# Optimization experiments

Hardware: AMD Instinct MI355X
Metric: run time of the kernel (lower is better)

Reference implementation:

```python
import jax, jax.numpy as jnp
import numpy as np

NR, NA = 2, 1                 # num_raw, num_angle
QDIM = NR + 2 * NA            # 4: [r, x1=cos(th), x2=sin(th)]
DQ = NR + NA                  # 3: [dr, dth]
D = 2 * NR + 3 * NA           # 7: full state dim
HID = 256
EPS = 1e-6


def setup_inputs() -> dict:
    key = jax.random.key(0)
    ks = jax.random.split(key, 4)
    B = 32768
    x = jax.random.normal(ks[0], (B, D), dtype=jnp.float32)
    W0 = jax.random.normal(ks[1], (HID, D), dtype=jnp.float32) / np.sqrt(D)
    b0 = jnp.zeros((HID,), dtype=jnp.float32)
    W1 = jax.random.normal(ks[2], (HID, HID), dtype=jnp.float32) / np.sqrt(HID)
    b1 = jnp.zeros((HID,), dtype=jnp.float32)
    W2 = jax.random.normal(ks[3], (1, HID), dtype=jnp.float32) / np.sqrt(HID)
    b2 = jnp.zeros((1,), dtype=jnp.float32)
    return {"x": x, "W0": W0, "b0": b0, "W1": W1, "b1": b1, "W2": W2, "b2": b2}


def _lnn_forward(x, W0, b0, W1, b1, W2, b2):
    def L_single(xi):  # scalar Lagrangian of one state (D,)
        h = jnp.tanh(W0 @ xi + b0)
        h = jnp.tanh(W1 @ h + b1)
        return (W2 @ h + b2)[0]

    grad_single = jax.grad(L_single)
    gradL = jax.vmap(grad_single)(x)                       # (B, D)

    # Rows of the Hessian corresponding to d/d(dr,dth): (B, DQ, D).
    # Replaces the torch per-row autograd.grad loop with one batched jacfwd.
    def g(xi):
        return grad_single(xi)[QDIM:]                      # dL/d(dr,dth), (DQ,)
    Hrows = jax.vmap(jax.jacfwd(g))(x)                     # (B, DQ, D)

    x1 = x[:, NR:NR + NA]                                  # cos part (B, NA)
    x2 = x[:, NR + NA:QDIM]                                # sin part (B, NA)

    Jr = Hrows[:, :, :NR]                                  # (B, DQ, NR)
    Jx1 = Hrows[:, :, NR:NR + NA]                          # (B, DQ, NA)
    Jx2 = Hrows[:, :, NR + NA:QDIM]                        # (B, DQ, NA)
    Hdq = Hrows[:, :, QDIM:] + EPS * jnp.eye(DQ, dtype=x.dtype)  # (B, DQ, DQ)

    # chain rule back to angle theta: d/dth = -x2 * d/dx1 + x1 * d/dx2
    Jth = -x2[:, None, :] * Jx1 + x1[:, None, :] * Jx2     # (B, DQ, NA)
    Jrth = jnp.concatenate([Jr, Jth], axis=2)              # (B, DQ, DQ)

    dLdr = gradL[:, :NR]
    dLdx1 = gradL[:, NR:NR + NA]
    dLdx2 = gradL[:, NR + NA:QDIM]
    dLdth = -x2 * dLdx1 + x1 * dLdx2
    dLdrdth = jnp.concatenate([dLdr, dLdth], axis=1)       # (B, DQ)

    dq = x[:, QDIM:]                                       # (B, DQ)
    dq_term = jnp.einsum('bij,bj->bi', Jrth, dq)

    rhs = dLdrdth - dq_term                                # control = 0 (no controlNet)
    ddq = jnp.linalg.solve(Hdq, rhs[..., None])[..., 0]    # (B, DQ)

    dr = dq[:, :NR]
    dth = dq[:, NR:]
    dx1 = -x2 * dth
    dx2 = x1 * dth
    return jnp.concatenate([dr, dx1, dx2, ddq], axis=1)    # (B, D)


def reference(x, W0, b0, W1, b1, W2, b2):
    return _lnn_forward(x, W0, b0, W1, b1, W2, b2)
```

## Files before the change

kernel.cpp:

```cpp
#include <hip/hip_runtime.h>
#include <math.h>

#define HID 256
#define EPS_REG 1e-6

typedef __attribute__((ext_vector_type(8))) short short8;
typedef __attribute__((ext_vector_type(4))) short short4v;
typedef __attribute__((ext_vector_type(4))) float v4f;

#define MFMA_BF16(a, b, c) __builtin_amdgcn_mfma_f32_16x16x32_bf16((a), (b), (c), 0, 0, 0)

__device__ __forceinline__ float fast_tanh(float z) {
    const float e = __expf(2.0f * z);
    const float d = e + 1.0f;
    float r = __builtin_amdgcn_rcpf(d);
    r = r * (2.0f - d * r);
    return fmaf(-2.0f, r, 1.0f);
}

__device__ __forceinline__ float rtn_bf16(float v, short* s) {
    unsigned r = (__float_as_uint(v) + 0x8000u) & 0xFFFF0000u;
    *s = (short)(r >> 16);
    return __uint_as_float(r);
}
__device__ __forceinline__ void split3(float v, short* a, short* b, short* c) {
    float f0 = rtn_bf16(v, a);
    float r1 = v - f0;
    float f1 = rtn_bf16(r1, b);
    float r2 = r1 - f1;
    (void)rtn_bf16(r2, c);
}

__global__ void prep_w1_frags(const float* __restrict__ W1, short* __restrict__ ws) {
    const int gid   = blockIdx.x * 128 + threadIdx.x;
    const int lane  = gid & 63;
    const int ks    = (gid >> 6) & 7;
    const int rt    = (gid >> 9) & 15;
    const int which = gid >> 13;
    const int m = lane & 15, q = lane >> 4;

    float v[8];
    if (which == 0) {
        const float* p = W1 + (size_t)(rt*16 + m)*HID + ks*32 + q*8;
        const float4 va = *(const float4*)(p);
        const float4 vb = *(const float4*)(p + 4);
        v[0]=va.x; v[1]=va.y; v[2]=va.z; v[3]=va.w;
        v[4]=vb.x; v[5]=vb.y; v[6]=vb.z; v[7]=vb.w;
    } else {
        const float* p = W1 + (size_t)(ks*32 + q*8)*HID + rt*16 + m;
#pragma unroll
        for (int t = 0; t < 8; ++t) v[t] = p[(size_t)t*HID];
    }
    short8 h8, m8, l8;
#pragma unroll
    for (int t = 0; t < 8; ++t) {
        short sh, sm, sl;
        split3(v[t], &sh, &sm, &sl);
        h8[t] = sh; m8[t] = sm; l8[t] = sl;
    }
    const size_t base = (size_t)which*3*65536 + ((size_t)(rt*8 + ks)*64 + lane)*8;
    *(short8*)(ws + base)          = h8;
    *(short8*)(ws + base + 65536)  = m8;
    *(short8*)(ws + base + 131072) = l8;
}

#define FRAG_NT_STRIDE 13056
#define FRAG_BUF_STRIDE 4352
#define BFRAG_SHORTS 26112
#define M0H_FLOATS 2304
#define PIPE_LDS_BYTES 122880

__device__ __forceinline__ void lnn_phase0(const float* __restrict__ x,
    const float* __restrict__ W0, const float* __restrict__ b0,
    int samp_base, short* __restrict__ Bf, float* __restrict__ M0, int tid)
{
    const int j  = tid & 255;
    const int s0 = (tid >> 8) * 4;
    float w0r[7];
#pragma unroll
    for (int d = 0; d < 7; ++d) w0r[d] = W0[j*7 + d];
    const float bj = b0[j];
    const int kbase = (j >> 3)*136 + (j & 7);
#pragma unroll
    for (int si = 0; si < 4; ++si) {
        const int s = s0 + si;
        const float* xs = x + (size_t)(samp_base + s)*7;
        float z = bj;
#pragma unroll
        for (int d = 0; d < 7; ++d) z = fmaf(w0r[d], xs[d], z);
        const float h  = fast_tanh(z);
        const float sg = 1.0f - h*h;
        M0[j*9 + s] = h;
        const int nt = s >> 2;
        const int cb = (s & 3) * 4;
        float vals[4] = {h, sg*w0r[4], sg*w0r[5], sg*w0r[6]};
#pragma unroll
        for (int comp = 0; comp < 4; ++comp) {
            short sh, sm, sl;
            split3(vals[comp], &sh, &sm, &sl);
            const int a = nt*FRAG_NT_STRIDE + kbase + (cb + comp)*8;
            Bf[a]                     = sh;
            Bf[a + FRAG_BUF_STRIDE]   = sm;
            Bf[a + 2*FRAG_BUF_STRIDE] = sl;
        }
    }
}

__device__ __forceinline__ void lnn_mm(const short8* __restrict__ Ah,
    const short8* __restrict__ Am, const short8* __restrict__ Al,
    const short* __restrict__ Bf, int w, int lane, int boff, v4f acc[2][2])
{
    short8 pah[2][2], pam[2][2], pal[2][2];
#pragma unroll
    for (int rtl = 0; rtl < 2; ++rtl) {
        const size_t fi = ((size_t)((w*2 + rtl)*8))*64 + lane;
        pah[0][rtl] = Ah[fi]; pam[0][rtl] = Am[fi]; pal[0][rtl] = Al[fi];
    }
#pragma unroll
    for (int ks = 0; ks < 8; ++ks) {
        const int cur = ks & 1, nxt = cur ^ 1;
        if (ks < 7) {
#pragma unroll
            for (int rtl = 0; rtl < 2; ++rtl) {
                const size_t fi = ((size_t)((w*2 + rtl)*8 + ks + 1))*64 + lane;
                pah[nxt][rtl] = Ah[fi]; pam[nxt][rtl] = Am[fi]; pal[nxt][rtl] = Al[fi];
            }
        }
        short8 bh[2], bm[2], bl[2];
#pragma unroll
        for (int nt = 0; nt < 2; ++nt) {
            const int a = nt*FRAG_NT_STRIDE + ks*544 + boff;
            bh[nt] = *(const short8*)(&Bf[a]);
            bm[nt] = *(const short8*)(&Bf[a + FRAG_BUF_STRIDE]);
            bl[nt] = *(const short8*)(&Bf[a + 2*FRAG_BUF_STRIDE]);
        }
#pragma unroll
        for (int rtl = 0; rtl < 2; ++rtl) {
            const short8 ah = pah[cur][rtl];
            const short8 am = pam[cur][rtl];
            const short8 al = pal[cur][rtl];
#pragma unroll
            for (int nt = 0; nt < 2; ++nt) {
                acc[rtl][nt] = MFMA_BF16(ah, bl[nt], acc[rtl][nt]);
                acc[rtl][nt] = MFMA_BF16(al, bh[nt], acc[rtl][nt]);
                acc[rtl][nt] = MFMA_BF16(am, bm[nt], acc[rtl][nt]);
                acc[rtl][nt] = MFMA_BF16(am, bh[nt], acc[rtl][nt]);
                acc[rtl][nt] = MFMA_BF16(ah, bm[nt], acc[rtl][nt]);
                acc[rtl][nt] = MFMA_BF16(ah, bh[nt], acc[rtl][nt]);
            }
        }
    }
}

__device__ __forceinline__ void lnn_epi1(v4f acc[2][2], short* __restrict__ Bf,
    const float* __restrict__ b1, const float* __restrict__ W2,
    int w, int lane, int q, int c)
{
    const int myreg = c & 3;
#pragma unroll
    for (int rtl = 0; rtl < 2; ++rtl) {
        const int base = (w*2 + rtl)*16;
        float b1r[4], w2r[4];
#pragma unroll
        for (int r = 0; r < 4; ++r) {
            b1r[r] = b1[base + q*4 + r];
            w2r[r] = W2[base + q*4 + r];
        }
        const int G  = (base >> 3) + (q >> 1);
        const int tq = (q & 1) * 4;
#pragma unroll
        for (int nt = 0; nt < 2; ++nt) {
            short4v ph, pm, pl;
#pragma unroll
            for (int r = 0; r < 4; ++r) {
                const float z0 = __shfl(acc[rtl][nt][r] + b1r[r], lane & ~3, 64);
                const float h1 = fast_tanh(z0);
                const float s1 = 1.0f - h1*h1;
                const float av = acc[rtl][nt][r];
                const float u  = (myreg == 0) ? (w2r[r]*s1)
                                              : (-2.0f*w2r[r]*h1*s1)*av;
                short sh, sm, sl;
                split3(u, &sh, &sm, &sl);
                ph[r] = sh; pm[r] = sm; pl[r] = sl;
            }
            const int a = nt*FRAG_NT_STRIDE + G*136 + c*8 + tq;
            *(short4v*)(&Bf[a])                     = ph;
            *(short4v*)(&Bf[a + FRAG_BUF_STRIDE])   = pm;
            *(short4v*)(&Bf[a + 2*FRAG_BUF_STRIDE]) = pl;
        }
    }
}

__device__ __forceinline__ void lnn_epi2(v4f acc2[2][2], short* __restrict__ Bf,
    const float* __restrict__ M0, const float* __restrict__ W0,
    int w, int lane, int q, int c)
{
    float* U0 = (float*)Bf;
#pragma unroll
    for (int rtl = 0; rtl < 2; ++rtl) {
#pragma unroll
        for (int reg = 0; reg < 4; ++reg) {
            const int j = (w*2 + rtl)*16 + q*4 + reg;
            const float w0sel = W0[j*7 + 3 + (c & 3)];
#pragma unroll
            for (int nt = 0; nt < 2; ++nt) {
                const int s = nt*4 + (c >> 2);
                const float pv = acc2[rtl][nt][reg];
                const float p0 = __shfl(pv, lane & ~3, 64);
                const float h0 = M0[j*9 + s];
                const float sg = 1.0f - h0*h0;
                const float t2 = -2.0f * p0 * h0 * sg;
                const float res = ((c & 3) == 0) ? (p0*sg)
                                                 : fmaf(pv, sg, t2 * w0sel);
                U0[j*36 + s*4 + (c & 3)] = res;
            }
        }
    }
}

__device__ __forceinline__ void lnn_phase3(const float* __restrict__ x,
    const float* __restrict__ W0, short* __restrict__ Bf,
    int samp_base, float* __restrict__ out, int w, int tid)
{
    const float* U0 = (const float*)Bf;
    float* scratch = ((float*)Bf) + 9216 + w * 425;
    const int t = tid & 63;
    float part[25];
#pragma unroll
    for (int qq = 0; qq < 25; ++qq) part[qq] = 0.0f;

#pragma unroll
    for (int m = 0; m < 4; ++m) {
        const int j = t + 64*m;
        const float4 uv = *(const float4*)(&U0[j*36 + w*4]);
        float w0d[7];
#pragma unroll
        for (int d = 0; d < 7; ++d) w0d[d] = W0[j*7 + d];
#pragma unroll
        for (int d = 0; d < 4; ++d) part[d] = fmaf(uv.x, w0d[d], part[d]);
#pragma unroll
        for (int d = 0; d < 7; ++d) {
            part[4  + d] = fmaf(uv.y, w0d[d], part[4  + d]);
            part[11 + d] = fmaf(uv.z, w0d[d], part[11 + d]);
            part[18 + d] = fmaf(uv.w, w0d[d], part[18 + d]);
        }
    }
#pragma unroll
    for (int off = 1; off <= 2; off <<= 1)
#pragma unroll
        for (int qq = 0; qq < 25; ++qq)
            part[qq] += __shfl_xor(part[qq], off, 64);
    {
        const int quad = t >> 2;
        if ((t & 3) == 0) {
#pragma unroll
            for (int e = 0; e < 25; ++e)
                scratch[e*17 + quad] = part[e];
        }
    }
    if (t < 25) {
        float tot = 0.0f;
#pragma unroll
        for (int k = 0; k < 16; ++k) tot += scratch[t*17 + k];
        scratch[t*17 + 16] = tot;
    }

    if (t == 0) {
        double g[25];
#pragma unroll
        for (int e = 0; e < 25; ++e) g[e] = (double)scratch[e*17 + 16];

        const float* xs = x + (size_t)(samp_base + w)*7;
        const double x1 = xs[2], x2 = xs[3];
        const double dq0 = xs[4], dq1 = xs[5], dth = xs[6];

        double M[3][3], rhs[3];
#pragma unroll
        for (int i = 0; i < 3; ++i) {
            const double J0 = g[4 + i*7 + 0];
            const double J1 = g[4 + i*7 + 1];
            const double J2 = -x2*g[4 + i*7 + 2] + x1*g[4 + i*7 + 3];
            const double dL = (i == 0) ? g[0]
                            : (i == 1) ? g[1]
                            : (-x2*g[2] + x1*g[3]);
            M[i][0] = g[4 + i*7 + 4] + (i == 0 ? EPS_REG : 0.0);
            M[i][1] = g[4 + i*7 + 5] + (i == 1 ? EPS_REG : 0.0);
            M[i][2] = g[4 + i*7 + 6] + (i == 2 ? EPS_REG : 0.0);
            rhs[i]  = dL - (J0*dq0 + J1*dq1 + J2*dth);
        }
        const double c00 = M[1][1]*M[2][2] - M[1][2]*M[2][1];
        const double c01 = M[1][2]*M[2][0] - M[1][0]*M[2][2];
        const double c02 = M[1][0]*M[2][1] - M[1][1]*M[2][0];
        const double det = M[0][0]*c00 + M[0][1]*c01 + M[0][2]*c02;
        const double inv = 1.0 / det;
        const double c10 = M[0][2]*M[2][1] - M[0][1]*M[2][2];
        const double c11 = M[0][0]*M[2][2] - M[0][2]*M[2][0];
        const double c12 = M[0][1]*M[2][0] - M[0][0]*M[2][1];
        const double c20 = M[0][1]*M[1][2] - M[0][2]*M[1][1];
        const double c21 = M[0][2]*M[1][0] - M[0][0]*M[1][2];
        const double c22 = M[0][0]*M[1][1] - M[0][1]*M[1][0];
        const double sol0 = (c00*rhs[0] + c10*rhs[1] + c20*rhs[2]) * inv;
        const double sol1 = (c01*rhs[0] + c11*rhs[1] + c21*rhs[2]) * inv;
        const double sol2 = (c02*rhs[0] + c12*rhs[1] + c22*rhs[2]) * inv;

        float* o = out + (size_t)(samp_base + w)*7;
        o[0] = (float)dq0;
        o[1] = (float)dq1;
        o[2] = (float)(-x2*dth);
        o[3] = (float)( x1*dth);
        o[4] = (float)sol0;
        o[5] = (float)sol1;
        o[6] = (float)sol2;
    }
}

__global__ __launch_bounds__(1024, 4)
void lnn_pipe(const float* __restrict__ x,
              const float* __restrict__ W0, const float* __restrict__ b0,
              const float* __restrict__ b1, const float* __restrict__ W2,
              const short* __restrict__ ws,
              float* __restrict__ out)
{
    extern __shared__ __align__(16) short smem[];

    const int tid  = threadIdx.x;
    const int w16  = tid >> 6;
    const int isA  = (w16 < 8) ? 1 : 0;
    const int w    = w16 & 7;
    const int lane = tid & 63;
    const int gtid = w*64 + lane;

    short* Bf = smem + (isA ? 0 : BFRAG_SHORTS);
    float* M0 = (float*)(smem + 2*BFRAG_SHORTS) + (isA ? 0 : M0H_FLOATS);
    const int samp0 = blockIdx.x * 16 + (isA ? 0 : 8);

    const short8* A1h = (const short8*)ws;
    const short8* A1m = A1h + 8192;
    const short8* A1l = A1h + 16384;
    const short8* A2h = A1h + 24576;
    const short8* A2m = A1h + 32768;
    const short8* A2l = A1h + 40960;

    const int q = lane >> 4;
    const int c = lane & 15;
    const int boff = q*136 + c*8;

    if (isA) lnn_phase0(x, W0, b0, samp0, Bf, M0, gtid);
    __syncthreads();

    v4f acc[2][2];
#pragma unroll
    for (int r = 0; r < 2; ++r)
#pragma unroll
        for (int n = 0; n < 2; ++n) acc[r][n] = (v4f){0.f, 0.f, 0.f, 0.f};
    if (isA) lnn_mm(A1h, A1m, A1l, Bf, w, lane, boff, acc);
    else     lnn_phase0(x, W0, b0, samp0, Bf, M0, gtid);
    __syncthreads();

    if (isA) lnn_epi1(acc, Bf, b1, W2, w, lane, q, c);
    else     lnn_mm(A1h, A1m, A1l, Bf, w, lane, boff, acc);
    __syncthreads();

    v4f acc2[2][2];
#pragma unroll
    for (int r = 0; r < 2; ++r)
#pragma unroll
        for (int n = 0; n < 2; ++n) acc2[r][n] = (v4f){0.f, 0.f, 0.f, 0.f};
    if (isA) lnn_mm(A2h, A2m, A2l, Bf, w, lane, boff, acc2);
    else     lnn_epi1(acc, Bf, b1, W2, w, lane, q, c);
    __syncthreads();

    if (isA) lnn_epi2(acc2, Bf, M0, W0, w, lane, q, c);
    else     lnn_mm(A2h, A2m, A2l, Bf, w, lane, boff, acc2);
    __syncthreads();

    if (isA) lnn_phase3(x, W0, Bf, samp0, out, w, gtid);
    else     lnn_epi2(acc2, Bf, M0, W0, w, lane, q, c);
    __syncthreads();

    if (!isA) lnn_phase3(x, W0, Bf, samp0, out, w, gtid);
}

__global__ __launch_bounds__(512, 4)
void lnn_mfma(const float* __restrict__ x,
              const float* __restrict__ W0, const float* __restrict__ b0,
              const float* __restrict__ b1, const float* __restrict__ W2,
              const short* __restrict__ ws,
              float* __restrict__ out)
{
    __shared__ __align__(16) short Bfrag[26112];
    __shared__ float M0h[HID * 9];

    const int tid   = threadIdx.x;
    const int samp0 = blockIdx.x * 8;
    const int lane  = tid & 63;
    const int w     = tid >> 6;

    lnn_phase0(x, W0, b0, samp0, Bfrag, M0h, tid);
    __syncthreads();

    const short8* A1h = (const short8*)ws;
    const short8* A1m = A1h + 8192;
    const short8* A1l = A1h + 16384;
    const short8* A2h = A1h + 24576;
    const short8* A2m = A1h + 32768;
    const short8* A2l = A1h + 40960;

    const int q = lane >> 4;
    const int c = lane & 15;
    const int boff = q*136 + c*8;

    v4f acc[2][2];
#pragma unroll
    for (int r = 0; r < 2; ++r)
#pragma unroll
        for (int n = 0; n < 2; ++n) acc[r][n] = (v4f){0.f, 0.f, 0.f, 0.f};
    lnn_mm(A1h, A1m, A1l, Bfrag, w, lane, boff, acc);
    __syncthreads();

    lnn_epi1(acc, Bfrag, b1, W2, w, lane, q, c);
    __syncthreads();

    v4f acc2[2][2];
#pragma unroll
    for (int r = 0; r < 2; ++r)
#pragma unroll
        for (int n = 0; n < 2; ++n) acc2[r][n] = (v4f){0.f, 0.f, 0.f, 0.f};
    lnn_mm(A2h, A2m, A2l, Bfrag, w, lane, boff, acc2);
    __syncthreads();

    lnn_epi2(acc2, Bfrag, M0h, W0, w, lane, q, c);
    __syncthreads();

    lnn_phase3(x, W0, Bfrag, samp0, out, w, tid);
}

#define TS8 8
#define SCP 36

__global__ void transpose_w1(const float* __restrict__ W1, float* __restrict__ W1T) {
    __shared__ float tile[32][33];
    const int bx = blockIdx.x & 7;
    const int by = blockIdx.x >> 3;
    const int tx = threadIdx.x & 31;
    const int ty = threadIdx.x >> 5;
#pragma unroll
    for (int q = 0; q < 4; ++q)
        tile[ty + q*8][tx] = W1[(by*32 + ty + q*8)*HID + bx*32 + tx];
    __syncthreads();
#pragma unroll
    for (int q = 0; q < 4; ++q)
        W1T[(bx*32 + ty + q*8)*HID + by*32 + tx] = tile[tx][ty + q*8];
}

__global__ __launch_bounds__(256, 2)
void lnn_fused(const float* __restrict__ x,
               const float* __restrict__ W0, const float* __restrict__ b0,
               const float* __restrict__ W1, const float* __restrict__ b1,
               const float* __restrict__ W2,
               const float* __restrict__ W1T, const int useT,
               float* __restrict__ out)
{
    __shared__ float M0[HID * SCP];
    __shared__ float U [HID * SCP];
    const int tid   = threadIdx.x;
    const int samp0 = blockIdx.x * TS8;
    {
        const int j = tid;
        float w0r[7];
#pragma unroll
        for (int d = 0; d < 7; ++d) w0r[d] = W0[j*7 + d];
        const float bj = b0[j];
#pragma unroll
        for (int s = 0; s < TS8; ++s) {
            const float* xs = x + (size_t)(samp0 + s)*7;
            float z = bj;
#pragma unroll
            for (int d = 0; d < 7; ++d) z = fmaf(w0r[d], xs[d], z);
            const float h  = tanhf(z);
            const float sg = 1.0f - h*h;
            float4 v = {h, sg * w0r[4], sg * w0r[5], sg * w0r[6]};
            *(float4*)(&M0[j*SCP + s*4]) = v;
        }
    }
    __syncthreads();
    const int it = tid & 63;
    const int ct = tid >> 6;
    float acc[4][8];
#pragma unroll
    for (int r = 0; r < 4; ++r)
#pragma unroll
        for (int c = 0; c < 8; ++c) acc[r][c] = 0.0f;
    if (useT) {
#pragma unroll 4
        for (int j = 0; j < HID; ++j) {
            const float4 w4 = *(const float4*)(W1T + (size_t)j*HID + it*4);
            const float4 ma = *(const float4*)(&M0[j*SCP + ct*8]);
            const float4 mb = *(const float4*)(&M0[j*SCP + ct*8 + 4]);
            const float w[4] = {w4.x, w4.y, w4.z, w4.w};
            const float m[8] = {ma.x, ma.y, ma.z, ma.w, mb.x, mb.y, mb.z, mb.w};
#pragma unroll
            for (int r = 0; r < 4; ++r)
#pragma unroll
                for (int c = 0; c < 8; ++c)
                    acc[r][c] = fmaf(w[r], m[c], acc[r][c]);
        }
    } else {
#pragma unroll 2
        for (int j = 0; j < HID; ++j) {
            float w[4];
#pragma unroll
            for (int r = 0; r < 4; ++r) w[r] = W1[(size_t)(it*4 + r)*HID + j];
            const float4 ma = *(const float4*)(&M0[j*SCP + ct*8]);
            const float4 mb = *(const float4*)(&M0[j*SCP + ct*8 + 4]);
            const float m[8] = {ma.x, ma.y, ma.z, ma.w, mb.x, mb.y, mb.z, mb.w};
#pragma unroll
            for (int r = 0; r < 4; ++r)
#pragma unroll
                for (int c = 0; c < 8; ++c)
                    acc[r][c] = fmaf(w[r], m[c], acc[r][c]);
        }
    }
    {
#pragma unroll
        for (int r = 0; r < 4; ++r) {
            const int i = it*4 + r;
            const float b1i = b1[i];
            const float w2i = W2[i];
#pragma unroll
            for (int cs = 0; cs < 2; ++cs) {
                const float z1 = acc[r][cs*4+0] + b1i;
                const float h1 = tanhf(z1);
                const float s1 = 1.0f - h1*h1;
                float4 uv;
                uv.x = w2i * s1;
                const float m2 = -2.0f * w2i * h1 * s1;
                uv.y = m2 * acc[r][cs*4+1];
                uv.z = m2 * acc[r][cs*4+2];
                uv.w = m2 * acc[r][cs*4+3];
                *(float4*)(&U[i*SCP + ct*8 + cs*4]) = uv;
            }
        }
    }
    __syncthreads();
    float acc2[4][8];
#pragma unroll
    for (int r = 0; r < 4; ++r)
#pragma unroll
        for (int c = 0; c < 8; ++c) acc2[r][c] = 0.0f;
#pragma unroll 4
    for (int i = 0; i < HID; ++i) {
        const float4 w4 = *(const float4*)(W1 + (size_t)i*HID + it*4);
        const float4 ua = *(const float4*)(&U[i*SCP + ct*8]);
        const float4 ub = *(const float4*)(&U[i*SCP + ct*8 + 4]);
        const float w[4] = {w4.x, w4.y, w4.z, w4.w};
        const float m[8] = {ua.x, ua.y, ua.z, ua.w, ub.x, ub.y, ub.z, ub.w};
#pragma unroll
        for (int r = 0; r < 4; ++r)
#pragma unroll
            for (int c = 0; c < 8; ++c)
                acc2[r][c] = fmaf(w[r], m[c], acc2[r][c]);
    }
    __syncthreads();
    {
#pragma unroll
        for (int r = 0; r < 4; ++r) {
            const int j = it*4 + r;
#pragma unroll
            for (int cs = 0; cs < 2; ++cs) {
                const int scb = ct*8 + cs*4;
                const float4 mm = *(const float4*)(&M0[j*SCP + scb]);
                const float h0v = mm.x;
                const float sg  = 1.0f - h0v*h0v;
                const float p   = acc2[r][cs*4+0];
                const float t2  = -2.0f * p * h0v;
                float4 uv;
                uv.x = p * sg;
                uv.y = fmaf(acc2[r][cs*4+1], sg, t2 * mm.y);
                uv.z = fmaf(acc2[r][cs*4+2], sg, t2 * mm.z);
                uv.w = fmaf(acc2[r][cs*4+3], sg, t2 * mm.w);
                *(float4*)(&U[j*SCP + scb]) = uv;
            }
        }
    }
    __syncthreads();
    const int s = tid >> 5;
    const int t = tid & 31;
    float part[25];
#pragma unroll
    for (int qq = 0; qq < 25; ++qq) part[qq] = 0.0f;
#pragma unroll
    for (int m = 0; m < 8; ++m) {
        const int j = t + 32*m;
        const float4 uv = *(const float4*)(&U[j*SCP + s*4]);
        float w0d[7];
#pragma unroll
        for (int d = 0; d < 7; ++d) w0d[d] = W0[j*7 + d];
#pragma unroll
        for (int d = 0; d < 4; ++d) part[d] = fmaf(uv.x, w0d[d], part[d]);
#pragma unroll
        for (int d = 0; d < 7; ++d) {
            part[4  + d] = fmaf(uv.y, w0d[d], part[4  + d]);
            part[11 + d] = fmaf(uv.z, w0d[d], part[11 + d]);
            part[18 + d] = fmaf(uv.w, w0d[d], part[18 + d]);
        }
    }
#pragma unroll
    for (int off = 16; off >= 1; off >>= 1)
#pragma unroll
        for (int qq = 0; qq < 25; ++qq)
            part[qq] += __shfl_xor(part[qq], off, 64);
    if (t == 0) {
        const float* xs = x + (size_t)(samp0 + s)*7;
        const double x1 = xs[2], x2 = xs[3];
        const double dq0 = xs[4], dq1 = xs[5], dth = xs[6];
        double A[3][4];
#pragma unroll
        for (int i = 0; i < 3; ++i) {
            const double J0 = part[4 + i*7 + 0];
            const double J1 = part[4 + i*7 + 1];
            const double J2 = -x2*(double)part[4 + i*7 + 2] + x1*(double)part[4 + i*7 + 3];
            const double dL = (i == 0) ? (double)part[0]
                            : (i == 1) ? (double)part[1]
                            : (-x2*(double)part[2] + x1*(double)part[3]);
            A[i][0] = (double)part[4 + i*7 + 4] + (i == 0 ? EPS_REG : 0.0);
            A[i][1] = (double)part[4 + i*7 + 5] + (i == 1 ? EPS_REG : 0.0);
            A[i][2] = (double)part[4 + i*7 + 6] + (i == 2 ? EPS_REG : 0.0);
            A[i][3] = dL - (J0*dq0 + J1*dq1 + J2*dth);
        }
        for (int cc = 0; cc < 2; ++cc) {
            int piv = cc;
            double mx = fabs(A[cc][cc]);
            for (int rr = cc + 1; rr < 3; ++rr) {
                const double v = fabs(A[rr][cc]);
                if (v > mx) { mx = v; piv = rr; }
            }
            if (piv != cc) {
                for (int k2 = 0; k2 < 4; ++k2) {
                    const double tmp = A[cc][k2]; A[cc][k2] = A[piv][k2]; A[piv][k2] = tmp;
                }
            }
            const double inv = 1.0 / A[cc][cc];
            for (int rr = cc + 1; rr < 3; ++rr) {
                const double f = A[rr][cc] * inv;
                for (int k2 = cc + 1; k2 < 4; ++k2) A[rr][k2] -= f * A[cc][k2];
            }
        }
        const double sol2 = A[2][3] / A[2][2];
        const double sol1 = (A[1][3] - A[1][2]*sol2) / A[1][1];
        const double sol0 = (A[0][3] - A[0][1]*sol1 - A[0][2]*sol2) / A[0][0];
        float* o = out + (size_t)(samp0 + s)*7;
        o[0] = (float)dq0;
        o[1] = (float)dq1;
        o[2] = (float)(-x2*dth);
        o[3] = (float)( x1*dth);
        o[4] = (float)sol0;
        o[5] = (float)sol1;
        o[6] = (float)sol2;
    }
}

extern "C" void kernel_launch(void* const* d_in, const int* in_sizes, int n_in,
                              void* d_out, int out_size, void* d_ws, size_t ws_size,
                              hipStream_t stream) {
    const float* x  = (const float*)d_in[0];
    const float* W0 = (const float*)d_in[1];
    const float* b0 = (const float*)d_in[2];
    const float* W1 = (const float*)d_in[3];
    const float* b1 = (const float*)d_in[4];
    const float* W2 = (const float*)d_in[5];
    float* out = (float*)d_out;

    const int B = in_sizes[0] / 7;
    const size_t NEED = 6u * 65536u * sizeof(short);

    static const bool big_lds_ok = [] {
        return hipFuncSetAttribute(reinterpret_cast<const void*>(lnn_pipe),
                                   hipFuncAttributeMaxDynamicSharedMemorySize,
                                   PIPE_LDS_BYTES) == hipSuccess;
    }();

    if (ws_size >= NEED && (B % 16) == 0 && big_lds_ok) {
        short* ws = (short*)d_ws;
        prep_w1_frags<<<128, 128, 0, stream>>>(W1, ws);
        lnn_pipe<<<B / 16, 1024, PIPE_LDS_BYTES, stream>>>(x, W0, b0, b1, W2, ws, out);
    } else if (ws_size >= NEED && (B % 8) == 0) {
        short* ws = (short*)d_ws;
        prep_w1_frags<<<128, 128, 0, stream>>>(W1, ws);
        lnn_mfma<<<B / 8, 512, 0, stream>>>(x, W0, b0, b1, W2, ws, out);
    } else {
        const int useT = (ws_size >= (size_t)HID * HID * sizeof(float)) ? 1 : 0;
        float* W1T = (float*)d_ws;
        if (useT) transpose_w1<<<64, 256, 0, stream>>>(W1, W1T);
        lnn_fused<<<B / TS8, 256, 0, stream>>>(x, W0, b0, W1, b1, W2, W1T, useT, out);
    }
}
```

Measured before the change: 305.6 us.

## Drop ping-pong pipe kernel, vectorize phase0, reorder MFMAs, dedupe tanh in epilogue

```diff
diff --git a/kernel.cpp b/kernel.cpp
--- a/kernel.cpp
+++ b/kernel.cpp
@@ -66,43 +66,51 @@
 
 #define FRAG_NT_STRIDE 13056
 #define FRAG_BUF_STRIDE 4352
-#define BFRAG_SHORTS 26112
-#define M0H_FLOATS 2304
-#define PIPE_LDS_BYTES 122880
 
 __device__ __forceinline__ void lnn_phase0(const float* __restrict__ x,
     const float* __restrict__ W0, const float* __restrict__ b0,
     int samp_base, short* __restrict__ Bf, float* __restrict__ M0, int tid)
 {
-    const int j  = tid & 255;
-    const int s0 = (tid >> 8) * 4;
-    float w0r[7];
-#pragma unroll
-    for (int d = 0; d < 7; ++d) w0r[d] = W0[j*7 + d];
-    const float bj = b0[j];
-    const int kbase = (j >> 3)*136 + (j & 7);
-#pragma unroll
-    for (int si = 0; si < 4; ++si) {
-        const int s = s0 + si;
-        const float* xs = x + (size_t)(samp_base + s)*7;
-        float z = bj;
-#pragma unroll
-        for (int d = 0; d < 7; ++d) z = fmaf(w0r[d], xs[d], z);
+    const int jq = tid & 63;
+    const int s  = tid >> 6;
+    const int j0 = jq * 4;
+    const float* xs = x + (size_t)(samp_base + s)*7;
+    float xv[7];
+#pragma unroll
+    for (int d = 0; d < 7; ++d) xv[d] = xs[d];
+    float4 wv[7];
+    const float* wp = W0 + (size_t)j0*7;
+#pragma unroll
+    for (int k = 0; k < 7; ++k) wv[k] = *(const float4*)(wp + 4*k);
+    const float* wf = (const float*)wv;
+    const int nt = s >> 2;
+    const int cb = (s & 3) * 4;
+    const int G  = j0 >> 3;
+    const int t0 = j0 & 7;
+    short4v hi4[4], mi4[4], lo4[4];
+#pragma unroll
+    for (int jj = 0; jj < 4; ++jj) {
+        const int j = j0 + jj;
+        float z = b0[j];
+#pragma unroll
+        for (int d = 0; d < 7; ++d) z = fmaf(wf[jj*7 + d], xv[d], z);
         const float h  = fast_tanh(z);
         const float sg = 1.0f - h*h;
         M0[j*9 + s] = h;
-        const int nt = s >> 2;
-        const int cb = (s & 3) * 4;
-        float vals[4] = {h, sg*w0r[4], sg*w0r[5], sg*w0r[6]};
+        float vals[4] = {h, sg*wf[jj*7 + 4], sg*wf[jj*7 + 5], sg*wf[jj*7 + 6]};
 #pragma unroll
         for (int comp = 0; comp < 4; ++comp) {
             short sh, sm, sl;
             split3(vals[comp], &sh, &sm, &sl);
-            const int a = nt*FRAG_NT_STRIDE + kbase + (cb + comp)*8;
-            Bf[a]                     = sh;
-            Bf[a + FRAG_BUF_STRIDE]   = sm;
-            Bf[a + 2*FRAG_BUF_STRIDE] = sl;
-        }
+            hi4[comp][jj] = sh; mi4[comp][jj] = sm; lo4[comp][jj] = sl;
+        }
+    }
+#pragma unroll
+    for (int comp = 0; comp < 4; ++comp) {
+        const int a = nt*FRAG_NT_STRIDE + G*136 + t0 + (cb + comp)*8;
+        *(short4v*)(&Bf[a])                     = hi4[comp];
+        *(short4v*)(&Bf[a + FRAG_BUF_STRIDE])   = mi4[comp];
+        *(short4v*)(&Bf[a + 2*FRAG_BUF_STRIDE]) = lo4[comp];
     }
 }
 
@@ -134,21 +142,38 @@
             bm[nt] = *(const short8*)(&Bf[a + FRAG_BUF_STRIDE]);
             bl[nt] = *(const short8*)(&Bf[a + 2*FRAG_BUF_STRIDE]);
         }
-#pragma unroll
-        for (int rtl = 0; rtl < 2; ++rtl) {
-            const short8 ah = pah[cur][rtl];
-            const short8 am = pam[cur][rtl];
-            const short8 al = pal[cur][rtl];
-#pragma unroll
-            for (int nt = 0; nt < 2; ++nt) {
-                acc[rtl][nt] = MFMA_BF16(ah, bl[nt], acc[rtl][nt]);
-                acc[rtl][nt] = MFMA_BF16(al, bh[nt], acc[rtl][nt]);
-                acc[rtl][nt] = MFMA_BF16(am, bm[nt], acc[rtl][nt]);
-                acc[rtl][nt] = MFMA_BF16(am, bh[nt], acc[rtl][nt]);
-                acc[rtl][nt] = MFMA_BF16(ah, bm[nt], acc[rtl][nt]);
-                acc[rtl][nt] = MFMA_BF16(ah, bh[nt], acc[rtl][nt]);
-            }
-        }
+        const short8 ah0 = pah[cur][0], ah1 = pah[cur][1];
+        const short8 am0 = pam[cur][0], am1 = pam[cur][1];
+        const short8 al0 = pal[cur][0], al1 = pal[cur][1];
+        acc[0][0] = MFMA_BF16(ah0, bl[0], acc[0][0]);
+        acc[0][1] = MFMA_BF16(ah0, bl[1], acc[0][1]);
+        acc[1][0] = MFMA_BF16(ah1, bl[0], acc[1][0]);
+        acc[1][1] = MFMA_BF16(ah1, bl[1], acc[1][1]);
+
+        acc[0][0] = MFMA_BF16(al0, bh[0], acc[0][0]);
+        acc[0][1] = MFMA_BF16(al0, bh[1], acc[0][1]);
+        acc[1][0] = MFMA_BF16(al1, bh[0], acc[1][0]);
+        acc[1][1] = MFMA_BF16(al1, bh[1], acc[1][1]);
+
+        acc[0][0] = MFMA_BF16(am0, bm[0], acc[0][0]);
+        acc[0][1] = MFMA_BF16(am0, bm[1], acc[0][1]);
+        acc[1][0] = MFMA_BF16(am1, bm[0], acc[1][0]);
+        acc[1][1] = MFMA_BF16(am1, bm[1], acc[1][1]);
+
+        acc[0][0] = MFMA_BF16(am0, bh[0], acc[0][0]);
+        acc[0][1] = MFMA_BF16(am0, bh[1], acc[0][1]);
+        acc[1][0] = MFMA_BF16(am1, bh[0], acc[1][0]);
+        acc[1][1] = MFMA_BF16(am1, bh[1], acc[1][1]);
+
+        acc[0][0] = MFMA_BF16(ah0, bm[0], acc[0][0]);
+        acc[0][1] = MFMA_BF16(ah0, bm[1], acc[0][1]);
+        acc[1][0] = MFMA_BF16(ah1, bm[0], acc[1][0]);
+        acc[1][1] = MFMA_BF16(ah1, bm[1], acc[1][1]);
+
+        acc[0][0] = MFMA_BF16(ah0, bh[0], acc[0][0]);
+        acc[0][1] = MFMA_BF16(ah0, bh[1], acc[0][1]);
+        acc[1][0] = MFMA_BF16(ah1, bh[0], acc[1][0]);
+        acc[1][1] = MFMA_BF16(ah1, bh[1], acc[1][1]);
     }
 }
 
@@ -157,6 +182,7 @@
     int w, int lane, int q, int c)
 {
     const int myreg = c & 3;
+    const int qbase = lane & ~3;
 #pragma unroll
     for (int rtl = 0; rtl < 2; ++rtl) {
         const int base = (w*2 + rtl)*16;
@@ -170,15 +196,27 @@
         const int tq = (q & 1) * 4;
 #pragma unroll
         for (int nt = 0; nt < 2; ++nt) {
+            const float zb0 = __shfl(acc[rtl][nt][0] + b1r[0], qbase, 64);
+            const float zb1 = __shfl(acc[rtl][nt][1] + b1r[1], qbase, 64);
+            const float zb2 = __shfl(acc[rtl][nt][2] + b1r[2], qbase, 64);
+            const float zb3 = __shfl(acc[rtl][nt][3] + b1r[3], qbase, 64);
+            const float zsel = (myreg == 0) ? zb0
+                             : (myreg == 1) ? zb1
+                             : (myreg == 2) ? zb2 : zb3;
+            const float ht = fast_tanh(zsel);
+            const float st = 1.0f - ht*ht;
+            float h1v[4], s1v[4];
+#pragma unroll
+            for (int r = 0; r < 4; ++r) {
+                h1v[r] = __shfl(ht, qbase + r, 64);
+                s1v[r] = __shfl(st, qbase + r, 64);
+            }
             short4v ph, pm, pl;
 #pragma unroll
             for (int r = 0; r < 4; ++r) {
-                const float z0 = __shfl(acc[rtl][nt][r] + b1r[r], lane & ~3, 64);
-                const float h1 = fast_tanh(z0);
-                const float s1 = 1.0f - h1*h1;
                 const float av = acc[rtl][nt][r];
-                const float u  = (myreg == 0) ? (w2r[r]*s1)
-                                              : (-2.0f*w2r[r]*h1*s1)*av;
+                const float u  = (myreg == 0) ? (w2r[r]*s1v[r])
+                                              : (-2.0f*w2r[r]*h1v[r]*s1v[r])*av;
                 short sh, sm, sl;
                 split3(u, &sh, &sm, &sl);
                 ph[r] = sh; pm[r] = sm; pl[r] = sl;
@@ -312,73 +350,6 @@
         o[5] = (float)sol1;
         o[6] = (float)sol2;
     }
-}
-
-__global__ __launch_bounds__(1024, 4)
-void lnn_pipe(const float* __restrict__ x,
-              const float* __restrict__ W0, const float* __restrict__ b0,
-              const float* __restrict__ b1, const float* __restrict__ W2,
-              const short* __restrict__ ws,
-              float* __restrict__ out)
-{
-    extern __shared__ __align__(16) short smem[];
-
-    const int tid  = threadIdx.x;
-    const int w16  = tid >> 6;
-    const int isA  = (w16 < 8) ? 1 : 0;
-    const int w    = w16 & 7;
-    const int lane = tid & 63;
-    const int gtid = w*64 + lane;
-
-    short* Bf = smem + (isA ? 0 : BFRAG_SHORTS);
-    float* M0 = (float*)(smem + 2*BFRAG_SHORTS) + (isA ? 0 : M0H_FLOATS);
-    const int samp0 = blockIdx.x * 16 + (isA ? 0 : 8);
-
-    const short8* A1h = (const short8*)ws;
-    const short8* A1m = A1h + 8192;
-    const short8* A1l = A1h + 16384;
-    const short8* A2h = A1h + 24576;
-    const short8* A2m = A1h + 32768;
-    const short8* A2l = A1h + 40960;
-
-    const int q = lane >> 4;
-    const int c = lane & 15;
-    const int boff = q*136 + c*8;
-
-    if (isA) lnn_phase0(x, W0, b0, samp0, Bf, M0, gtid);
-    __syncthreads();
-
-    v4f acc[2][2];
-#pragma unroll
-    for (int r = 0; r < 2; ++r)
-#pragma unroll
-        for (int n = 0; n < 2; ++n) acc[r][n] = (v4f){0.f, 0.f, 0.f, 0.f};
-    if (isA) lnn_mm(A1h, A1m, A1l, Bf, w, lane, boff, acc);
-    else     lnn_phase0(x, W0, b0, samp0, Bf, M0, gtid);
-    __syncthreads();
-
-    if (isA) lnn_epi1(acc, Bf, b1, W2, w, lane, q, c);
-    else     lnn_mm(A1h, A1m, A1l, Bf, w, lane, boff, acc);
-    __syncthreads();
-
-    v4f acc2[2][2];
-#pragma unroll
-    for (int r = 0; r < 2; ++r)
-#pragma unroll
-        for (int n = 0; n < 2; ++n) acc2[r][n] = (v4f){0.f, 0.f, 0.f, 0.f};
-    if (isA) lnn_mm(A2h, A2m, A2l, Bf, w, lane, boff, acc2);
-    else     lnn_epi1(acc, Bf, b1, W2, w, lane, q, c);
-    __syncthreads();
-
-    if (isA) lnn_epi2(acc2, Bf, M0, W0, w, lane, q, c);
-    else     lnn_mm(A2h, A2m, A2l, Bf, w, lane, boff, acc2);
-    __syncthreads();
-
-    if (isA) lnn_phase3(x, W0, Bf, samp0, out, w, gtid);
-    else     lnn_epi2(acc2, Bf, M0, W0, w, lane, q, c);
-    __syncthreads();
-
-    if (!isA) lnn_phase3(x, W0, Bf, samp0, out, w, gtid);
 }
 
 __global__ __launch_bounds__(512, 4)
@@ -674,17 +645,7 @@
     const int B = in_sizes[0] / 7;
     const size_t NEED = 6u * 65536u * sizeof(short);
 
-    static const bool big_lds_ok = [] {
-        return hipFuncSetAttribute(reinterpret_cast<const void*>(lnn_pipe),
-                                   hipFuncAttributeMaxDynamicSharedMemorySize,
-                                   PIPE_LDS_BYTES) == hipSuccess;
-    }();
-
-    if (ws_size >= NEED && (B % 16) == 0 && big_lds_ok) {
-        short* ws = (short*)d_ws;
-        prep_w1_frags<<<128, 128, 0, stream>>>(W1, ws);
-        lnn_pipe<<<B / 16, 1024, PIPE_LDS_BYTES, stream>>>(x, W0, b0, b1, W2, ws, out);
-    } else if (ws_size >= NEED && (B % 8) == 0) {
+    if (ws_size >= NEED && (B % 8) == 0) {
         short* ws = (short*)d_ws;
         prep_w1_frags<<<128, 128, 0, stream>>>(W1, ws);
         lnn_mfma<<<B / 8, 512, 0, stream>>>(x, W0, b0, b1, W2, ws, out);
```

New measurement: 276.0 us. 9.7% less time.
